# Performance work log

Hardware: AMD Instinct MI355X
Metric: run time of the kernel (lower is better)

## Reference

```python
import jax, jax.numpy as jnp
import numpy as np
from jax import lax

VOCAB = 50000
EMB = 256
HID = 512          # bidirectional output dim
H = HID // 2       # per-direction hidden size
B = 32
T = 1024
K = 14             # 12 entities + START + STOP
START = K - 2
STOP = K - 1


def setup_inputs() -> dict:
    key = jax.random.key(0)
    ks = jax.random.split(key, 16)
    rn = lambda k, shape, s=0.05: (jax.random.normal(k, shape, jnp.float32) * s)
    crf = jax.random.normal(ks[14], (K, K), jnp.float32)
    # forbid transitions into START and out of STOP (as in torch init)
    crf = crf.at[:, START].set(-1000.0).at[STOP, :].set(-1000.0)
    return {
        "sentences": jax.random.randint(ks[0], (B, T), 0, VOCAB),
        "emb": rn(ks[1], (VOCAB, EMB), 1.0),
        "Wih_f": rn(ks[2], (4 * H, EMB)), "Whh_f": rn(ks[3], (4 * H, H)),
        "bih_f": rn(ks[4], (4 * H,)), "bhh_f": rn(ks[5], (4 * H,)),
        "Wih_b": rn(ks[6], (4 * H, EMB)), "Whh_b": rn(ks[7], (4 * H, H)),
        "bih_b": rn(ks[8], (4 * H,)), "bhh_b": rn(ks[9], (4 * H,)),
        "h0": rn(ks[10], (2, B, H), 1.0),  # [dir, B, H] like torch init_hidden randn
        "c0": rn(ks[11], (2, B, H), 1.0),
        "W_out": rn(ks[12], (K, HID)), "b_out": rn(ks[13], (K,)),
        "crf": crf,
    }


def _lstm_dir(x, h0, c0, Wih, Whh, bih, bhh, reverse):
    # x: [B, T, E] -> hs: [B, T, H]; PyTorch gate order i, f, g, o
    def step(carry, xt):
        h, c = carry
        g = xt @ Wih.T + bih + h @ Whh.T + bhh  # [B, 4H]
        i, f, gg, o = jnp.split(g, 4, axis=-1)
        c = jax.nn.sigmoid(f) * c + jax.nn.sigmoid(i) * jnp.tanh(gg)
        h = jax.nn.sigmoid(o) * jnp.tanh(c)
        return (h, c), h
    _, hs = lax.scan(step, (h0, c0), jnp.swapaxes(x, 0, 1), reverse=reverse)
    return jnp.swapaxes(hs, 0, 1)


def _viterbi(logits, crf):
    # logits: [T, K]; max-plus recurrence over time
    def step(prev, lt):
        v = prev[:, None] + crf          # [K, K]: from-tag x to-tag
        return lt + jnp.max(v, axis=0), jnp.argmax(v, axis=0)
    last, bps = lax.scan(step, logits[0], logits[1:])  # bps: [T-1, K]
    score = jnp.max(last)
    last_tag = jnp.argmax(last)
    def back(tag, bp):
        p = bp[tag]
        return p, p
    _, rest = lax.scan(back, last_tag, bps, reverse=True)  # path[0..T-2]
    path = jnp.concatenate([rest, last_tag[None]])
    return score, path


def reference(sentences, emb, Wih_f, Whh_f, bih_f, bhh_f,
              Wih_b, Whh_b, bih_b, bhh_b, h0, c0, W_out, b_out, crf):
    x = emb[sentences]  # [B, T, E]
    hf = _lstm_dir(x, h0[0], c0[0], Wih_f, Whh_f, bih_f, bhh_f, False)
    hb = _lstm_dir(x, h0[1], c0[1], Wih_b, Whh_b, bih_b, bhh_b, True)
    hs = jnp.concatenate([hf, hb], axis=-1)        # [B, T, HID]
    logits = hs @ W_out.T + b_out                  # [B, T, K]
    scores, paths = jax.vmap(lambda l: _viterbi(l, crf))(logits)
    return scores, paths
```

## Files before the change

### kernel.cpp

```cpp
#include <hip/hip_runtime.h>
#include <hip/hip_bf16.h>
#include <cstdint>

#define B_ 32
#define T_ 1024
#define E_ 256
#define H_ 256
#define G_ 1024
#define NTAG 14
#define LOG2E 1.4426950408889634f

typedef __bf16 bf8_t __attribute__((ext_vector_type(8)));
typedef float f4_t __attribute__((ext_vector_type(4)));
typedef int i4_t __attribute__((ext_vector_type(4)));
typedef unsigned short u16x4 __attribute__((ext_vector_type(4)));

__device__ __forceinline__ unsigned short f2bf(float f) {
    unsigned u = __builtin_bit_cast(unsigned, f);
    u = u + 0x7FFFu + ((u >> 16) & 1u);
    return (unsigned short)(u >> 16);
}
__device__ __forceinline__ float bf2f(unsigned short s) {
    unsigned u = ((unsigned)s) << 16;
    return __builtin_bit_cast(float, u);
}
__device__ __forceinline__ float fexp2(float x) { return __builtin_amdgcn_exp2f(x); }
__device__ __forceinline__ float frcp(float x) { return __builtin_amdgcn_rcpf(x); }
__device__ __forceinline__ float sigf(float x) {
    return frcp(1.0f + fexp2(-LOG2E * x));
}
__device__ __forceinline__ float tanh2_(float x) {
    return 1.0f - 2.0f * frcp(fexp2((2.0f * LOG2E) * x) + 1.0f);
}
__device__ __forceinline__ f4_t mfma16(bf8_t a, bf8_t b, f4_t c) {
    return __builtin_amdgcn_mfma_f32_16x16x32_bf16(a, b, c, 0, 0, 0);
}

__global__ __launch_bounds__(256) void setup_kernel(
        const int* sent, const float* emb,
        const float* whh_f, const float* whh_b,
        const float* wih_f, const float* wih_b,
        const float* bih_f, const float* bhh_f,
        const float* bih_b, const float* bhh_b,
        const float* wout,
        unsigned short* xbf, signed char* qw, float* sw,
        unsigned short* wih_bf, float* biasc, unsigned short* wout_bf) {
    int bid = blockIdx.x, thr = threadIdx.x;
    if (bid < 8192) {
        int tid = bid * 256 + thr;
        int bt = tid >> 6;
        int e0 = (tid & 63) << 2;
        int tok = sent[bt];
        float4 v = *reinterpret_cast<const float4*>(emb + (size_t)tok * E_ + e0);
        u16x4 o;
        o[0] = f2bf(v.x); o[1] = f2bf(v.y); o[2] = f2bf(v.z); o[3] = f2bf(v.w);
        *reinterpret_cast<u16x4*>(xbf + (size_t)bt * E_ + e0) = o;
        return;
    }
    if (bid < 8704) {
        int row = (bid - 8192) * 4 + (thr >> 6);
        int l = thr & 63;
        int d = row >> 10, rr = row & 1023;
        const float* src = (d ? whh_b : whh_f) + (size_t)rr * 256;
        float4 v = *reinterpret_cast<const float4*>(src + 4 * l);
        float am = fmaxf(fmaxf(fabsf(v.x), fabsf(v.y)), fmaxf(fabsf(v.z), fabsf(v.w)));
#pragma unroll
        for (int off = 1; off < 64; off <<= 1)
            am = fmaxf(am, __shfl_xor(am, off));
        am = fmaxf(am, 1e-20f);
        float inv = 127.f / am;
        int q0 = (int)__builtin_rintf(v.x * inv), q1 = (int)__builtin_rintf(v.y * inv);
        int q2 = (int)__builtin_rintf(v.z * inv), q3 = (int)__builtin_rintf(v.w * inv);
        unsigned u = (q0 & 255) | ((q1 & 255) << 8) | ((q2 & 255) << 16) | ((q3 & 255) << 24);
        *reinterpret_cast<unsigned*>(qw + (size_t)row * 256 + 4 * l) = u;
        if (l == 0) sw[row] = am / 127.f;
        return;
    }
    int tid = (bid - 8704) * 256 + thr;
    if (tid < 524288) {
        int d = tid >> 18, off = tid & 262143;
        wih_bf[tid] = f2bf((d ? wih_b : wih_f)[off]);
        return;
    }
    int t2 = tid - 524288;
    if (t2 < 8192) {
        int n = t2 >> 9, k = t2 & 511;
        wout_bf[t2] = (n < NTAG) ? f2bf(wout[n * 512 + k]) : (unsigned short)0;
        return;
    }
    int t3 = t2 - 8192;
    if (t3 < 2048) {
        int d = t3 >> 10, g = t3 & 1023;
        biasc[t3] = d ? (bih_b[g] + bhh_b[g]) : (bih_f[g] + bhh_f[g]);
    }
}

__global__ __launch_bounds__(256, 1) void xproj_kernel(const unsigned short* xbf,
        const unsigned short* wih_bf, const float* biasc, unsigned short* xg4) {
    int tt = blockIdx.x;
    int y = blockIdx.y;
    int ns = y & 3, bh = (y >> 2) & 1, d = y >> 3;
    int w = threadIdx.x >> 6, l = threadIdx.x & 63;
    int l15 = l & 15, lgp = l >> 4;
    __shared__ unsigned short sh[256][16];

    int nbase = ns * 256 + w * 64;
    const unsigned short* wd = wih_bf + (size_t)d * 262144;
    bf8_t breg[4][8];
    float bias[4];
#pragma unroll
    for (int p = 0; p < 4; ++p) {
        int n = nbase + 16 * p + l15;
        bias[p] = biasc[d * G_ + n];
        const unsigned short* brow = wd + (size_t)n * E_ + 8 * lgp;
#pragma unroll
        for (int ks = 0; ks < 8; ++ks)
            breg[p][ks] = *reinterpret_cast<const bf8_t*>(brow + 32 * ks);
    }
#pragma unroll
    for (int p = 0; p < 4; ++p)
#pragma unroll
        for (int ks = 0; ks < 8; ++ks)
            asm volatile("" : "+v"(breg[p][ks]));

    const unsigned short* arow =
        xbf + ((size_t)(16 * bh + l15) * 1024 + tt * 16) * E_ + 8 * lgp;

    for (int it = 0; it < 16; ++it) {
        int t = tt * 16 + it;
        bf8_t a[8];
#pragma unroll
        for (int ks = 0; ks < 8; ++ks)
            a[ks] = *reinterpret_cast<const bf8_t*>(arow + 32 * ks);
        arow += 256;

        f4_t acc[4];
#pragma unroll
        for (int p = 0; p < 4; ++p) { acc[p][0] = 0.f; acc[p][1] = 0.f; acc[p][2] = 0.f; acc[p][3] = 0.f; }
#pragma unroll
        for (int p = 0; p < 4; ++p)
#pragma unroll
            for (int ks = 0; ks < 8; ++ks)
                acc[p] = mfma16(a[ks], breg[p][ks], acc[p]);

#pragma unroll
        for (int p = 0; p < 4; ++p)
#pragma unroll
            for (int r = 0; r < 4; ++r)
                sh[w * 64 + 16 * p + l15][4 * lgp + r] = f2bf(acc[p][r] + bias[p]);
        __syncthreads();
        int q = threadIdx.x;
#pragma unroll
        for (int p = 0; p < 8; ++p) {
            int b2g = 8 * bh + p;
            size_t base = ((size_t)(d * 16 + b2g) * 1024 + t) * 2048 + ns * 256 + q;
            xg4[base]        = sh[q][2 * p];
            xg4[base + 1024] = sh[q][2 * p + 1];
        }
        __syncthreads();
    }
}

__global__ __launch_bounds__(512, 2) void lstm_kernel(const unsigned short* xg4,
        const signed char* qw, const float* sw, const float* h0, const float* c0,
        unsigned short* hs) {
    int bid = blockIdx.x;
    int b2 = bid & 15, d = bid >> 4;
    int tid = threadIdx.x;
    int w = tid >> 6, l = tid & 63, l15 = l & 15, lgp = l >> 4;

    __shared__ __attribute__((aligned(16))) signed char h8[2][2][320];
    __shared__ float red_sh[8];

    const signed char* qwd = qw + (size_t)d * 262144;

    i4_t wreg[4][2][4];
#pragma unroll
    for (int gt = 0; gt < 4; ++gt)
#pragma unroll
        for (int jt = 0; jt < 2; ++jt) {
            int n = 256 * gt + 32 * w + 16 * jt + l15;
#pragma unroll
            for (int ks = 0; ks < 4; ++ks)
                wreg[gt][jt][ks] = *reinterpret_cast<const i4_t*>(
                    qwd + (size_t)n * 256 + 64 * ks + 16 * lgp);
        }
#pragma unroll
    for (int gt = 0; gt < 4; ++gt)
#pragma unroll
        for (int jt = 0; jt < 2; ++jt)
#pragma unroll
            for (int ks = 0; ks < 4; ++ks)
                asm volatile("" : "+v"(wreg[gt][jt][ks]));

    int jt_c = lgp & 1, m_c = lgp >> 1;
    int j = 32 * w + 16 * jt_c + l15;

    float swv[4];
#pragma unroll
    for (int gt = 0; gt < 4; ++gt)
        swv[gt] = sw[d * 1024 + 256 * gt + j];
    float c = c0[((size_t)d * 32 + b2 * 2 + m_c) * 256 + j];

    int im = tid >> 8, ij = tid & 255;
    float v0 = h0[((size_t)d * 32 + b2 * 2 + im) * 256 + ij];
    float am = fabsf(v0);
#pragma unroll
    for (int off = 1; off < 64; off <<= 1)
        am = fmaxf(am, __shfl_xor(am, off));
    if (l == 0) red_sh[w] = am;
    __syncthreads();
    float bmax = red_sh[0];
#pragma unroll
    for (int q = 1; q < 8; ++q) bmax = fmaxf(bmax, red_sh[q]);
    bmax = fmaxf(bmax, 1e-20f);
    float s0 = bmax / 127.f;
    h8[1][im][ij] = (signed char)(int)__builtin_rintf(v0 * (127.f / bmax));

    float dq[4];
#pragma unroll
    for (int gt = 0; gt < 4; ++gt) dq[gt] = swv[gt] * s0;

    int t0 = d ? 1023 : 0;
    int xinc = d ? -2048 : 2048;
    int hinc = d ? -512 : 512;
    const unsigned short* xq = xg4 + ((size_t)(d * 16 + b2) * 1024 + t0) * 2048
                               + m_c * 1024 + j;
    unsigned short* hsp = hs + ((size_t)(b2 * 2 + m_c) * 1024 + t0) * 512 + d * 256 + j;

    unsigned short xc[4], xn[4];
#pragma unroll
    for (int gt = 0; gt < 4; ++gt) xc[gt] = xq[256 * gt];

    i4_t z4 = (i4_t){0, 0, 0, 0};
    asm volatile("" : "+v"(z4));

    __syncthreads();

    for (int s = 0; s < 1024; ++s) {
        int rp = (s + 1) & 1, wp = s & 1;

        if (s < 1023) {
            xq += xinc;
#pragma unroll
            for (int gt = 0; gt < 4; ++gt) xn[gt] = xq[256 * gt];
        }

        i4_t a[4];
#pragma unroll
        for (int ks = 0; ks < 4; ++ks)
            a[ks] = *reinterpret_cast<const i4_t*>(&h8[rp][l15 & 1][64 * ks + 16 * lgp]);

        i4_t acc[4][2];
#pragma unroll
        for (int gt = 0; gt < 4; ++gt)
#pragma unroll
            for (int jt = 0; jt < 2; ++jt) {
                acc[gt][jt] = __builtin_amdgcn_mfma_i32_16x16x64_i8(
                    a[0], wreg[gt][jt][0], z4, 0, 0, 0);
#pragma unroll
                for (int ks = 1; ks < 4; ++ks)
                    acc[gt][jt] = __builtin_amdgcn_mfma_i32_16x16x64_i8(
                        a[ks], wreg[gt][jt][ks], acc[gt][jt], 0, 0, 0);
            }

        int gi[4];
#pragma unroll
        for (int gt = 0; gt < 4; ++gt) {
            int e0 = jt_c ? acc[gt][1][0] : acc[gt][0][0];
            int e1 = jt_c ? acc[gt][1][1] : acc[gt][0][1];
            gi[gt] = m_c ? e1 : e0;
        }

        float pi = dq[0] * (float)gi[0] + bf2f(xc[0]);
        float pf = dq[1] * (float)gi[1] + bf2f(xc[1]);
        float pg = dq[2] * (float)gi[2] + bf2f(xc[2]);
        float po = dq[3] * (float)gi[3] + bf2f(xc[3]);
        float iv = sigf(pi), fv = sigf(pf), ov = sigf(po);
        float gv = tanh2_(pg);
        float cn = fv * c + iv * gv;
        c = cn;
        float hv = ov * tanh2_(cn);
        *hsp = f2bf(hv);
        hsp += hinc;
        h8[wp][m_c][j] = (signed char)(int)__builtin_rintf(hv * 127.f);

        if (s == 0) {
#pragma unroll
            for (int gt = 0; gt < 4; ++gt) dq[gt] = swv[gt] * (1.f / 127.f);
        }
#pragma unroll
        for (int gt = 0; gt < 4; ++gt) xc[gt] = xn[gt];

        asm volatile("s_waitcnt lgkmcnt(0)" ::: "memory");
        __builtin_amdgcn_sched_barrier(0);
        __builtin_amdgcn_s_barrier();
    }
}

__global__ __launch_bounds__(256) void viterbi_kernel(const unsigned short* hs,
        const unsigned short* wout_bf, const float* b_out, const float* crf,
        float* out) {
    int b = blockIdx.x;
    int tid = threadIdx.x;
    int ww = tid >> 6, l = tid & 63, l15 = l & 15, lgp = l >> 4;

    __shared__ float lg[1024][16];
    __shared__ unsigned char bp[1024][16];
    __shared__ unsigned char pth[1024];

    float bo = (l15 < NTAG) ? b_out[l15] : 0.0f;
    const unsigned short* brow = wout_bf + (size_t)l15 * 512 + 8 * lgp;
    for (int k = 0; k < 16; ++k) {
        int mt = ww + 4 * k;
        const unsigned short* arow = hs + ((size_t)b * 1024 + mt * 16 + l15) * 512 + 8 * lgp;
        f4_t acc; acc[0] = 0.f; acc[1] = 0.f; acc[2] = 0.f; acc[3] = 0.f;
#pragma unroll
        for (int ks = 0; ks < 16; ++ks) {
            bf8_t a = *reinterpret_cast<const bf8_t*>(arow + 32 * ks);
            bf8_t bb = *reinterpret_cast<const bf8_t*>(brow + 32 * ks);
            acc = mfma16(a, bb, acc);
        }
#pragma unroll
        for (int r = 0; r < 4; ++r)
            lg[mt * 16 + 4 * lgp + r][l15] = acc[r] + bo;
    }
    __syncthreads();

    if (ww == 0) {
        int j = l;
        float crfj[NTAG];
#pragma unroll
        for (int i = 0; i < NTAG; ++i)
            crfj[i] = (j < NTAG) ? crf[i * NTAG + j] : 0.0f;
        float v = (j < NTAG) ? lg[0][j] : -3.0e38f;
        for (int t = 1; t < 1024; ++t) {
            float sv[NTAG];
#pragma unroll
            for (int i = 0; i < NTAG; ++i)
                sv[i] = __shfl(v, i) + crfj[i];
            float m0 = fmaxf(fmaxf(sv[0], sv[1]), sv[2]);
            float m1 = fmaxf(fmaxf(sv[3], sv[4]), sv[5]);
            float m2 = fmaxf(fmaxf(sv[6], sv[7]), sv[8]);
            float m3 = fmaxf(fmaxf(sv[9], sv[10]), sv[11]);
            float m4 = fmaxf(sv[12], sv[13]);
            float best = fmaxf(fmaxf(fmaxf(m0, m1), fmaxf(m2, m3)), m4);
            unsigned msk = 0;
#pragma unroll
            for (int i = 0; i < NTAG; ++i)
                msk |= (sv[i] == best) ? (1u << i) : 0u;
            int arg = __builtin_ctz(msk);
            float lt = (j < NTAG) ? lg[t][j] : 0.0f;
            v = (j < NTAG) ? (lt + best) : -3.0e38f;
            if (j < 16) bp[t][j] = (unsigned char)arg;
        }
        float best = -3.0e38f; int tag = 0;
#pragma unroll
        for (int jj = 0; jj < NTAG; ++jj) {
            float s = __shfl(v, jj);
            if (s > best) { best = s; tag = jj; }
        }
        if (j == 0) {
            out[b] = best;
            int tg = tag;
            pth[1023] = (unsigned char)tg;
            for (int t = 1023; t >= 1; --t) {
                tg = bp[t][tg];
                pth[t - 1] = (unsigned char)tg;
            }
        }
    }
    __syncthreads();
    float* pout = out + 32 + (size_t)b * 1024;
    for (int t = tid; t < 1024; t += 256)
        pout[t] = (float)pth[t];
}

extern "C" void kernel_launch(void* const* d_in, const int* in_sizes, int n_in,
                              void* d_out, int out_size, void* d_ws, size_t ws_size,
                              hipStream_t stream) {
    const int* sent = (const int*)d_in[0];
    const float* emb = (const float*)d_in[1];
    const float* wih_f = (const float*)d_in[2];
    const float* whh_f = (const float*)d_in[3];
    const float* bih_f = (const float*)d_in[4];
    const float* bhh_f = (const float*)d_in[5];
    const float* wih_b = (const float*)d_in[6];
    const float* whh_b = (const float*)d_in[7];
    const float* bih_b = (const float*)d_in[8];
    const float* bhh_b = (const float*)d_in[9];
    const float* h0 = (const float*)d_in[10];
    const float* c0 = (const float*)d_in[11];
    const float* wout = (const float*)d_in[12];
    const float* b_out = (const float*)d_in[13];
    const float* crf = (const float*)d_in[14];

    char* ws = (char*)d_ws;
    signed char* qw       = (signed char*)(ws + 0);
    float* sw             = (float*)(ws + 524288);
    unsigned short* wih_bf = (unsigned short*)(ws + 1048576);
    float* biasc          = (float*)(ws + 2097152);
    unsigned short* wout_bf = (unsigned short*)(ws + 2105344);
    unsigned short* xbf   = (unsigned short*)(ws + 2121728);
    unsigned short* xg4   = (unsigned short*)(ws + 18898944);
    unsigned short* hs    = (unsigned short*)(ws + 153116672);
    float* out = (float*)d_out;

    hipLaunchKernelGGL(setup_kernel, dim3(10792), dim3(256), 0, stream,
                       sent, emb, whh_f, whh_b, wih_f, wih_b,
                       bih_f, bhh_f, bih_b, bhh_b, wout,
                       xbf, qw, sw, wih_bf, biasc, wout_bf);
    hipLaunchKernelGGL(xproj_kernel, dim3(64, 16), dim3(256), 0, stream,
                       xbf, wih_bf, biasc, xg4);
    hipLaunchKernelGGL(lstm_kernel, dim3(32), dim3(512), 0, stream,
                       xg4, qw, sw, h0, c0, hs);
    hipLaunchKernelGGL(viterbi_kernel, dim3(32), dim3(256), 0, stream,
                       hs, wout_bf, b_out, crf, out);
}
```

Baseline: 1.168 ms.

## Fold setup preprocessing into xproj and viterbi kernels, dropping setup launch

Removes the separate setup kernel. The embedding gather, the bf16 conversion of Wih and the bias sum now happen inside xproj, which reads fp32 embeddings and weights directly. The Whh int8 quantisation moves into extra blocks of the xproj grid, and the W_out bf16 conversion moves into the viterbi kernel's registers. This saves a launch and the round trip of the intermediate bf16 buffers, at the cost of redundant fp32 loads and conversions of weights and embeddings in each xproj block.

```diff
diff --git a/kernel.cpp b/kernel.cpp
--- a/kernel.cpp
+++ b/kernel.cpp
@@ -14,6 +14,7 @@
 typedef float f4_t __attribute__((ext_vector_type(4)));
 typedef int i4_t __attribute__((ext_vector_type(4)));
 typedef unsigned short u16x4 __attribute__((ext_vector_type(4)));
+typedef unsigned short u16x8 __attribute__((ext_vector_type(8)));
 
 __device__ __forceinline__ unsigned short f2bf(float f) {
     unsigned u = __builtin_bit_cast(unsigned, f);
@@ -24,6 +25,16 @@
     unsigned u = ((unsigned)s) << 16;
     return __builtin_bit_cast(float, u);
 }
+__device__ __forceinline__ bf8_t cvt8(float4 x, float4 y) {
+    u16x8 u;
+    u[0] = f2bf(x.x); u[1] = f2bf(x.y); u[2] = f2bf(x.z); u[3] = f2bf(x.w);
+    u[4] = f2bf(y.x); u[5] = f2bf(y.y); u[6] = f2bf(y.z); u[7] = f2bf(y.w);
+    return __builtin_bit_cast(bf8_t, u);
+}
+__device__ __forceinline__ bf8_t zero8() {
+    u16x8 z = {0, 0, 0, 0, 0, 0, 0, 0};
+    return __builtin_bit_cast(bf8_t, z);
+}
 __device__ __forceinline__ float fexp2(float x) { return __builtin_amdgcn_exp2f(x); }
 __device__ __forceinline__ float frcp(float x) { return __builtin_amdgcn_rcpf(x); }
 __device__ __forceinline__ float sigf(float x) {
@@ -36,30 +47,19 @@
     return __builtin_amdgcn_mfma_f32_16x16x32_bf16(a, b, c, 0, 0, 0);
 }
 
-__global__ __launch_bounds__(256) void setup_kernel(
+__global__ __launch_bounds__(256, 1) void xproj_kernel(
         const int* sent, const float* emb,
-        const float* whh_f, const float* whh_b,
         const float* wih_f, const float* wih_b,
         const float* bih_f, const float* bhh_f,
         const float* bih_b, const float* bhh_b,
-        const float* wout,
-        unsigned short* xbf, signed char* qw, float* sw,
-        unsigned short* wih_bf, float* biasc, unsigned short* wout_bf) {
-    int bid = blockIdx.x, thr = threadIdx.x;
-    if (bid < 8192) {
-        int tid = bid * 256 + thr;
-        int bt = tid >> 6;
-        int e0 = (tid & 63) << 2;
-        int tok = sent[bt];
-        float4 v = *reinterpret_cast<const float4*>(emb + (size_t)tok * E_ + e0);
-        u16x4 o;
-        o[0] = f2bf(v.x); o[1] = f2bf(v.y); o[2] = f2bf(v.z); o[3] = f2bf(v.w);
-        *reinterpret_cast<u16x4*>(xbf + (size_t)bt * E_ + e0) = o;
-        return;
-    }
-    if (bid < 8704) {
-        int row = (bid - 8192) * 4 + (thr >> 6);
-        int l = thr & 63;
+        const float* whh_f, const float* whh_b,
+        unsigned short* xg4, signed char* qw, float* sw) {
+    int bid = blockIdx.x;
+    int thr = threadIdx.x;
+    int l = thr & 63, l15 = l & 15, lgp = l >> 4;
+
+    if (bid >= 1024) {
+        int row = (bid - 1024) * 4 + (thr >> 6);
         int d = row >> 10, rr = row & 1023;
         const float* src = (d ? whh_b : whh_f) + (size_t)rr * 256;
         float4 v = *reinterpret_cast<const float4*>(src + 4 * l);
@@ -76,46 +76,30 @@
         if (l == 0) sw[row] = am / 127.f;
         return;
     }
-    int tid = (bid - 8704) * 256 + thr;
-    if (tid < 524288) {
-        int d = tid >> 18, off = tid & 262143;
-        wih_bf[tid] = f2bf((d ? wih_b : wih_f)[off]);
-        return;
-    }
-    int t2 = tid - 524288;
-    if (t2 < 8192) {
-        int n = t2 >> 9, k = t2 & 511;
-        wout_bf[t2] = (n < NTAG) ? f2bf(wout[n * 512 + k]) : (unsigned short)0;
-        return;
-    }
-    int t3 = t2 - 8192;
-    if (t3 < 2048) {
-        int d = t3 >> 10, g = t3 & 1023;
-        biasc[t3] = d ? (bih_b[g] + bhh_b[g]) : (bih_f[g] + bhh_f[g]);
-    }
-}
-
-__global__ __launch_bounds__(256, 1) void xproj_kernel(const unsigned short* xbf,
-        const unsigned short* wih_bf, const float* biasc, unsigned short* xg4) {
-    int tt = blockIdx.x;
-    int y = blockIdx.y;
+
+    int tt = bid & 63;
+    int y = bid >> 6;
     int ns = y & 3, bh = (y >> 2) & 1, d = y >> 3;
-    int w = threadIdx.x >> 6, l = threadIdx.x & 63;
-    int l15 = l & 15, lgp = l >> 4;
+    int w = thr >> 6;
     __shared__ unsigned short sh[256][16];
 
     int nbase = ns * 256 + w * 64;
-    const unsigned short* wd = wih_bf + (size_t)d * 262144;
+    const float* wd = (d ? wih_b : wih_f);
+    const float* bihd = d ? bih_b : bih_f;
+    const float* bhhd = d ? bhh_b : bhh_f;
     bf8_t breg[4][8];
     float bias[4];
 #pragma unroll
     for (int p = 0; p < 4; ++p) {
         int n = nbase + 16 * p + l15;
-        bias[p] = biasc[d * G_ + n];
-        const unsigned short* brow = wd + (size_t)n * E_ + 8 * lgp;
-#pragma unroll
-        for (int ks = 0; ks < 8; ++ks)
-            breg[p][ks] = *reinterpret_cast<const bf8_t*>(brow + 32 * ks);
+        bias[p] = bihd[n] + bhhd[n];
+        const float* brow = wd + (size_t)n * E_ + 8 * lgp;
+#pragma unroll
+        for (int ks = 0; ks < 8; ++ks) {
+            float4 x = *reinterpret_cast<const float4*>(brow + 32 * ks);
+            float4 z = *reinterpret_cast<const float4*>(brow + 32 * ks + 4);
+            breg[p][ks] = cvt8(x, z);
+        }
     }
 #pragma unroll
     for (int p = 0; p < 4; ++p)
@@ -123,16 +107,20 @@
         for (int ks = 0; ks < 8; ++ks)
             asm volatile("" : "+v"(breg[p][ks]));
 
-    const unsigned short* arow =
-        xbf + ((size_t)(16 * bh + l15) * 1024 + tt * 16) * E_ + 8 * lgp;
+    int row16 = 16 * bh + l15;
+    const int* sent_row = sent + (size_t)row16 * 1024 + tt * 16;
 
     for (int it = 0; it < 16; ++it) {
         int t = tt * 16 + it;
+        int tok = sent_row[it];
+        const float* erow = emb + (size_t)tok * E_ + 8 * lgp;
         bf8_t a[8];
 #pragma unroll
-        for (int ks = 0; ks < 8; ++ks)
-            a[ks] = *reinterpret_cast<const bf8_t*>(arow + 32 * ks);
-        arow += 256;
+        for (int ks = 0; ks < 8; ++ks) {
+            float4 x = *reinterpret_cast<const float4*>(erow + 32 * ks);
+            float4 z = *reinterpret_cast<const float4*>(erow + 32 * ks + 4);
+            a[ks] = cvt8(x, z);
+        }
 
         f4_t acc[4];
 #pragma unroll
@@ -149,7 +137,7 @@
             for (int r = 0; r < 4; ++r)
                 sh[w * 64 + 16 * p + l15][4 * lgp + r] = f2bf(acc[p][r] + bias[p]);
         __syncthreads();
-        int q = threadIdx.x;
+        int q = thr;
 #pragma unroll
         for (int p = 0; p < 8; ++p) {
             int b2g = 8 * bh + p;
@@ -299,7 +287,7 @@
 }
 
 __global__ __launch_bounds__(256) void viterbi_kernel(const unsigned short* hs,
-        const unsigned short* wout_bf, const float* b_out, const float* crf,
+        const float* wout, const float* b_out, const float* crf,
         float* out) {
     int b = blockIdx.x;
     int tid = threadIdx.x;
@@ -310,7 +298,18 @@
     __shared__ unsigned char pth[1024];
 
     float bo = (l15 < NTAG) ? b_out[l15] : 0.0f;
-    const unsigned short* brow = wout_bf + (size_t)l15 * 512 + 8 * lgp;
+    bf8_t brow[16];
+#pragma unroll
+    for (int ks = 0; ks < 16; ++ks) {
+        if (l15 < NTAG) {
+            const float* wr = wout + (size_t)l15 * 512 + 32 * ks + 8 * lgp;
+            float4 x = *reinterpret_cast<const float4*>(wr);
+            float4 z = *reinterpret_cast<const float4*>(wr + 4);
+            brow[ks] = cvt8(x, z);
+        } else {
+            brow[ks] = zero8();
+        }
+    }
     for (int k = 0; k < 16; ++k) {
         int mt = ww + 4 * k;
         const unsigned short* arow = hs + ((size_t)b * 1024 + mt * 16 + l15) * 512 + 8 * lgp;
@@ -318,8 +317,7 @@
 #pragma unroll
         for (int ks = 0; ks < 16; ++ks) {
             bf8_t a = *reinterpret_cast<const bf8_t*>(arow + 32 * ks);
-            bf8_t bb = *reinterpret_cast<const bf8_t*>(brow + 32 * ks);
-            acc = mfma16(a, bb, acc);
+            acc = mfma16(a, brow[ks], acc);
         }
 #pragma unroll
         for (int r = 0; r < 4; ++r)
@@ -398,22 +396,15 @@
     char* ws = (char*)d_ws;
     signed char* qw       = (signed char*)(ws + 0);
     float* sw             = (float*)(ws + 524288);
-    unsigned short* wih_bf = (unsigned short*)(ws + 1048576);
-    float* biasc          = (float*)(ws + 2097152);
-    unsigned short* wout_bf = (unsigned short*)(ws + 2105344);
-    unsigned short* xbf   = (unsigned short*)(ws + 2121728);
     unsigned short* xg4   = (unsigned short*)(ws + 18898944);
     unsigned short* hs    = (unsigned short*)(ws + 153116672);
     float* out = (float*)d_out;
 
-    hipLaunchKernelGGL(setup_kernel, dim3(10792), dim3(256), 0, stream,
-                       sent, emb, whh_f, whh_b, wih_f, wih_b,
-                       bih_f, bhh_f, bih_b, bhh_b, wout,
-                       xbf, qw, sw, wih_bf, biasc, wout_bf);
-    hipLaunchKernelGGL(xproj_kernel, dim3(64, 16), dim3(256), 0, stream,
-                       xbf, wih_bf, biasc, xg4);
+    hipLaunchKernelGGL(xproj_kernel, dim3(1536), dim3(256), 0, stream,
+                       sent, emb, wih_f, wih_b, bih_f, bhh_f, bih_b, bhh_b,
+                       whh_f, whh_b, xg4, qw, sw);
     hipLaunchKernelGGL(lstm_kernel, dim3(32), dim3(512), 0, stream,
                        xg4, qw, sw, h0, c0, hs);
     hipLaunchKernelGGL(viterbi_kernel, dim3(32), dim3(256), 0, stream,
-                       hs, wout_bf, b_out, crf, out);
-}
+                       hs, wout, b_out, crf, out);
+}
```

After: 1.222 ms. 4.6% more time.
